# Optimization experiments

Hardware: AMD Instinct MI355X
Metric: run time of the kernel (lower is better)

The kernel has to match this reference:

```python
import jax, jax.numpy as jnp
import numpy as np

MAX_DEGREE = 7  # selected_degree for every neuron (== config.max_degree)


def _cheb_combine(alpha, coeffs):
    """sum_d coeffs[:, d] * T_d(alpha) via the Chebyshev recurrence.

    alpha:  [B, out]
    coeffs: [out, D+1]
    returns [B, out]
    """
    t_m2 = jnp.ones_like(alpha)          # T_0
    t_m1 = alpha                          # T_1
    acc = coeffs[:, 0] + coeffs[:, 1] * alpha

    def body(carry, c_d):                 # c_d: [out]
        tm2, tm1, a = carry
        t = 2.0 * alpha * tm1 - tm2       # T_d recurrence
        return (tm1, t, a + c_d * t), None

    (_, _, acc), _ = jax.lax.scan(body, (t_m2, t_m1, acc), coeffs[:, 2:].T)
    return acc


def _kan_layer(x, w, b, coeffs, cW, cb):
    # w: [out, in] (stacked per-neuron projection vectors), b: [out]
    alpha = x @ w.T + b                   # [B, out] -- per-neuron scalar projection
    neuron_out = _cheb_combine(alpha, coeffs)  # [B, out]
    return neuron_out @ cW + cb           # combine_W [out,out], combin_b [out]


def setup_inputs() -> dict:
    key = jax.random.key(0)
    ks = jax.random.split(key, 12)
    B = 16384
    shape = [1024, 1024, 256]
    D1 = MAX_DEGREE + 1
    inp = {"x": jax.random.normal(ks[0], (B, shape[0]), dtype=jnp.float32)}
    ki = 1
    for li, (din, dout) in enumerate(zip(shape[:-1], shape[1:]), start=1):
        inp[f"w{li}"] = jax.random.normal(ks[ki], (dout, din), dtype=jnp.float32) / np.sqrt(din); ki += 1
        inp[f"b{li}"] = jnp.zeros((dout,), dtype=jnp.float32)
        inp[f"coeffs{li}"] = jax.random.normal(ks[ki], (dout, D1), dtype=jnp.float32) * 0.1; ki += 1
        inp[f"cW{li}"] = jnp.eye(dout, dtype=jnp.float32)
        inp[f"cb{li}"] = jnp.zeros((dout,), dtype=jnp.float32)
    return inp


def reference(x, w1, b1, coeffs1, cW1, cb1, w2, b2, coeffs2, cW2, cb2):
    h = _kan_layer(x, w1, b1, coeffs1, cW1, cb1)
    return _kan_layer(h, w2, b2, coeffs2, cW2, cb2)
```

## Files before the change

### kernel.cpp

```cpp
#include <hip/hip_runtime.h>


typedef __attribute__((ext_vector_type(8))) short short8;
typedef __attribute__((ext_vector_type(4))) float f32x4;
typedef unsigned short ushort_t;

#define GAS(p) ((const __attribute__((address_space(1))) void*)(p))
#define LAS(p) ((__attribute__((address_space(3))) void*)(p))

__device__ __forceinline__ void split2(float f, ushort_t& h, ushort_t& l) {
    const unsigned u = __float_as_uint(f);
    h = (ushort_t)(u >> 16);
    const float hf = __uint_as_float(u & 0xFFFF0000u);
    l = (ushort_t)(__float_as_uint(f - hf) >> 16);
}

__global__ __launch_bounds__(256)
void fused_split(const float* __restrict__ x, ushort_t* __restrict__ xh, ushort_t* __restrict__ xl,
                 const float* __restrict__ w1, ushort_t* __restrict__ w1h, ushort_t* __restrict__ w1l) {
    const int bid = blockIdx.x;
    const float* src; ushort_t* hi; ushort_t* lo; int i;
    if (bid < 16384) { src = x;  hi = xh;  lo = xl;  i = bid * 256 + threadIdx.x; }
    else             { src = w1; hi = w1h; lo = w1l; i = (bid - 16384) * 256 + threadIdx.x; }
    const float4 v = ((const float4*)src)[i];
    ushort4 h, l;
    split2(v.x, h.x, l.x); split2(v.y, h.y, l.y);
    split2(v.z, h.z, l.z); split2(v.w, h.w, l.w);
    ((ushort4*)hi)[i] = h;
    ((ushort4*)lo)[i] = l;
}

constexpr int PKT = 16;
__global__ __launch_bounds__(256)
void prep_gemm_sk(const float* __restrict__ A, const float* __restrict__ W,
                  float* __restrict__ Cp, int M, int N, int K, int KS) {
    __shared__ float As[PKT][68];
    __shared__ float Bs[PKT][68];
    const int tid = threadIdx.x;
    const int bn = blockIdx.x, bm = blockIdx.y, bz = blockIdx.z;
    const int kc = K / KS, k0 = bz * kc;
    const int tx = tid & 15, ty = tid >> 4;
    float acc[4][4];
#pragma unroll
    for (int i = 0; i < 4; ++i)
#pragma unroll
        for (int j = 0; j < 4; ++j) acc[i][j] = 0.f;
    const float* Ab = A + (size_t)(bm * 64) * K + k0;
    const float* Wb = W + (size_t)(bn * 64) * K + k0;
    const int sr = tid >> 2;
    const int sc = (tid & 3) * 4;
    for (int kt = 0; kt < kc; kt += PKT) {
        const float4 va = *(const float4*)(Ab + (size_t)sr * K + kt + sc);
        As[sc + 0][sr] = va.x; As[sc + 1][sr] = va.y; As[sc + 2][sr] = va.z; As[sc + 3][sr] = va.w;
        const float4 vb = *(const float4*)(Wb + (size_t)sr * K + kt + sc);
        Bs[sc + 0][sr] = vb.x; Bs[sc + 1][sr] = vb.y; Bs[sc + 2][sr] = vb.z; Bs[sc + 3][sr] = vb.w;
        __syncthreads();
#pragma unroll
        for (int k = 0; k < PKT; ++k) {
            const float4 a4 = *(const float4*)&As[k][ty * 4];
            const float4 b4 = *(const float4*)&Bs[k][tx * 4];
            const float a[4] = {a4.x, a4.y, a4.z, a4.w};
            const float b[4] = {b4.x, b4.y, b4.z, b4.w};
#pragma unroll
            for (int i = 0; i < 4; ++i)
#pragma unroll
                for (int j = 0; j < 4; ++j) acc[i][j] = fmaf(a[i], b[j], acc[i][j]);
        }
        __syncthreads();
    }
    float* Cb = Cp + (size_t)bz * M * N + (size_t)(bm * 64 + ty * 4) * N + bn * 64 + tx * 4;
#pragma unroll
    for (int i = 0; i < 4; ++i)
        *(float4*)(Cb + (size_t)i * N) = make_float4(acc[i][0], acc[i][1], acc[i][2], acc[i][3]);
}

__global__ __launch_bounds__(256)
void prep_small(const float* __restrict__ m2p, ushort_t* __restrict__ m2h, ushort_t* __restrict__ m2l,
                const float* __restrict__ cW2, ushort_t* __restrict__ cw2h, ushort_t* __restrict__ cw2l,
                const float* __restrict__ cb1, const float* __restrict__ w2,
                const float* __restrict__ b2, float* __restrict__ b2e) {
    const int bid = blockIdx.x;
    if (bid < 256) {
        const int i = bid * 256 + threadIdx.x;
        float4 s = ((const float4*)m2p)[i];
#pragma unroll
        for (int z = 1; z < 4; ++z) {
            const float4 v = ((const float4*)m2p)[(size_t)z * 65536 + i];
            s.x += v.x; s.y += v.y; s.z += v.z; s.w += v.w;
        }
        ushort4 h, l;
        split2(s.x, h.x, l.x); split2(s.y, h.y, l.y);
        split2(s.z, h.z, l.z); split2(s.w, h.w, l.w);
        ((ushort4*)m2h)[i] = h;
        ((ushort4*)m2l)[i] = l;
    } else if (bid < 512) {
        const int i = (bid - 256) * 256 + threadIdx.x;
        const int r = i >> 8, c = i & 255;
        ushort_t h, l;
        split2(cW2[r * 256 + c], h, l);
        cw2h[c * 256 + r] = h;
        cw2l[c * 256 + r] = l;
    } else {
        const int wave = threadIdx.x >> 6, lane = threadIdx.x & 63;
        const int n = (bid - 512) * 4 + wave;
        const float4* row = (const float4*)(w2 + (size_t)n * 1024);
        const float4* c4  = (const float4*)cb1;
        float s = 0.f;
#pragma unroll
        for (int i = 0; i < 4; ++i) {
            const int idx = lane + i * 64;
            const float4 a = row[idx], c = c4[idx];
            s += a.x * c.x + a.y * c.y + a.z * c.z + a.w * c.w;
        }
#pragma unroll
        for (int off = 32; off; off >>= 1) s += __shfl_down(s, off);
        if (lane == 0) b2e[n] = s + b2[n];
    }
}

__global__ __launch_bounds__(512, 2)
void kan_mfma256(const ushort_t* __restrict__ Ahg,
                 const ushort_t* __restrict__ Alg,
                 const ushort_t* __restrict__ Bhg,
                 const ushort_t* __restrict__ Blg,
                 const float* __restrict__ bias,
                 const float* __restrict__ coeffs,
                 ushort_t* __restrict__ Chh,
                 ushort_t* __restrict__ Chl,
                 int M, int N, int K)
{
    __shared__ __align__(16) ushort_t LDS[2][4][256 * 32];

    const int tid  = threadIdx.x;
    const int lane = tid & 63;
    const int wave = tid >> 6;

    const int gx  = gridDim.x;
    const int nwg = gx * gridDim.y;
    int wg = blockIdx.y * gx + blockIdx.x;
    wg = (wg & 7) * (nwg >> 3) + (wg >> 3);
    const int bn = wg % gx;
    const int bm = wg / gx;

    const int wm = wave >> 2;
    const int wn = wave & 3;
    const int lr = lane & 15;
    const int lg = lane >> 4;

    const int sg  = wave & 3;
    const int r0a = (wave >> 2) * 128;
    const size_t aRow0 = (size_t)bm * 256;
    const size_t bRow0 = (size_t)bn * 256;

    f32x4 acc[8][4];
#pragma unroll
    for (int m = 0; m < 8; ++m)
#pragma unroll
        for (int n = 0; n < 4; ++n) acc[m][n] = f32x4{0.f, 0.f, 0.f, 0.f};

    auto stage = [&](int s, int kt) {
#pragma unroll
        for (int rc = 0; rc < 2; ++rc) {
            const int r0 = r0a + rc * 64;
            const size_t ga = (aRow0 + r0 + lane) * K + kt + sg * 8;
            const size_t gb = (bRow0 + r0 + lane) * K + kt + sg * 8;
            const int di = sg * 2048 + r0 * 8;
            __builtin_amdgcn_global_load_lds(GAS(Ahg + ga), LAS(&LDS[s][0][di]), 16, 0, 0);
            __builtin_amdgcn_global_load_lds(GAS(Alg + ga), LAS(&LDS[s][1][di]), 16, 0, 0);
            __builtin_amdgcn_global_load_lds(GAS(Bhg + gb), LAS(&LDS[s][2][di]), 16, 0, 0);
            __builtin_amdgcn_global_load_lds(GAS(Blg + gb), LAS(&LDS[s][3][di]), 16, 0, 0);
        }
    };

    stage(0, 0);
    asm volatile("s_waitcnt vmcnt(0)" ::: "memory");
    __builtin_amdgcn_s_barrier();

    const int nt = K >> 5;

#define CLUSTER256(MH)                                                          \
    {                                                                           \
        short8 ah[4], al4[4];                                                   \
        _Pragma("unroll")                                                       \
        for (int m = 0; m < 4; ++m) {                                           \
            const int idx = lg * 2048 + (wm * 128 + (MH) * 64 + m * 16 + lr) * 8;\
            ah[m]  = *(const short8*)&LDS[cur][0][idx];                         \
            al4[m] = *(const short8*)&LDS[cur][1][idx];                         \
        }                                                                       \
        asm volatile("s_waitcnt lgkmcnt(0)" ::: "memory");                      \
        __builtin_amdgcn_sched_barrier(0);                                      \
        __builtin_amdgcn_s_setprio(1);                                          \
        _Pragma("unroll")                                                       \
        for (int m = 0; m < 4; ++m)                                             \
            _Pragma("unroll")                                                   \
            for (int n = 0; n < 4; ++n) {                                       \
                acc[(MH)*4+m][n] = __builtin_amdgcn_mfma_f32_16x16x32_bf16(ah[m],  bh[n], acc[(MH)*4+m][n], 0, 0, 0); \
                acc[(MH)*4+m][n] = __builtin_amdgcn_mfma_f32_16x16x32_bf16(ah[m],  bl[n], acc[(MH)*4+m][n], 0, 0, 0); \
                acc[(MH)*4+m][n] = __builtin_amdgcn_mfma_f32_16x16x32_bf16(al4[m], bh[n], acc[(MH)*4+m][n], 0, 0, 0); \
            }                                                                   \
        __builtin_amdgcn_s_setprio(0);                                          \
    }

    for (int t = 0; t < nt; ++t) {
        const int cur = t & 1;
        const bool more = (t + 1) < nt;

        if (more) stage(cur ^ 1, (t + 1) << 5);

        short8 bh[4], bl[4];
#pragma unroll
        for (int n = 0; n < 4; ++n) {
            const int idx = lg * 2048 + (wn * 64 + n * 16 + lr) * 8;
            bh[n] = *(const short8*)&LDS[cur][2][idx];
            bl[n] = *(const short8*)&LDS[cur][3][idx];
        }
        CLUSTER256(0)
        CLUSTER256(1)

        if (more) {
            asm volatile("s_waitcnt vmcnt(0)" ::: "memory");
            __builtin_amdgcn_s_barrier();
        }
    }
#undef CLUSTER256

    const int gm0 = bm * 256 + wm * 128;
    const int gn0 = bn * 256 + wn * 64;
#pragma unroll
    for (int n = 0; n < 4; ++n) {
        const int colg = gn0 + n * 16 + lr;
        const float bia = bias[colg];
        float cf[8];
        {
            const float4 u0 = *(const float4*)(coeffs + (size_t)colg * 8);
            const float4 u1 = *(const float4*)(coeffs + (size_t)colg * 8 + 4);
            cf[0] = u0.x; cf[1] = u0.y; cf[2] = u0.z; cf[3] = u0.w;
            cf[4] = u1.x; cf[5] = u1.y; cf[6] = u1.z; cf[7] = u1.w;
        }
#pragma unroll
        for (int m = 0; m < 8; ++m) {
            const int rowb = gm0 + m * 16 + lg * 4;
#pragma unroll
            for (int j = 0; j < 4; ++j) {
                const float alpha = acc[m][n][j] + bia;
                float tm2 = 1.f, tm1 = alpha;
                float v = fmaf(cf[1], alpha, cf[0]);
#pragma unroll
                for (int d = 2; d < 8; ++d) {
                    const float tch = 2.f * alpha * tm1 - tm2;
                    v = fmaf(cf[d], tch, v);
                    tm2 = tm1; tm1 = tch;
                }
                const size_t o = (size_t)(rowb + j) * N + colg;
                ushort_t h, l2;
                split2(v, h, l2);
                Chh[o] = h; Chl[o] = l2;
            }
        }
    }
}

template<bool CHEB, bool OUT_F32>
__global__ __launch_bounds__(256, 2)
void kan_mfma(const ushort_t* __restrict__ Ahg,
              const ushort_t* __restrict__ Alg,
              const ushort_t* __restrict__ Bhg,
              const ushort_t* __restrict__ Blg,
              const float* __restrict__ bias,
              const float* __restrict__ coeffs,
              float* __restrict__ Cf,
              ushort_t* __restrict__ Chh,
              ushort_t* __restrict__ Chl,
              int M, int N, int K)
{
    __shared__ __align__(16) ushort_t LDS[2][4][128 * 32];

    const int tid  = threadIdx.x;
    const int lane = tid & 63;
    const int wave = tid >> 6;

    const int gx = gridDim.x;
    const int nwg = gx * gridDim.y;
    int wg = blockIdx.y * gx + blockIdx.x;
    wg = (wg & 7) * (nwg >> 3) + (wg >> 3);
    const int bn = wg % gx;
    const int bm = wg / gx;

    const int wm = wave >> 1, wn = wave & 1;
    const int lr = lane & 15;
    const int lg = lane >> 4;

    f32x4 acc[4][4];
#pragma unroll
    for (int m = 0; m < 4; ++m)
#pragma unroll
        for (int n = 0; n < 4; ++n) acc[m][n] = f32x4{0.f, 0.f, 0.f, 0.f};

    const size_t aRow0 = (size_t)(bm * 128);
    const size_t bRow0 = (size_t)(bn * 128);
    const int sg = wave;
    const int ldsb = sg * 1024;

    auto stage = [&](int s, int kt) {
#pragma unroll
        for (int rc = 0; rc < 2; ++rc) {
            const int r0 = rc * 64;
            const size_t ga = (aRow0 + r0 + lane) * K + kt + sg * 8;
            const size_t gb = (bRow0 + r0 + lane) * K + kt + sg * 8;
            const int di = ldsb + r0 * 8;
            __builtin_amdgcn_global_load_lds(GAS(Ahg + ga), LAS(&LDS[s][0][di]), 16, 0, 0);
            __builtin_amdgcn_global_load_lds(GAS(Alg + ga), LAS(&LDS[s][1][di]), 16, 0, 0);
            __builtin_amdgcn_global_load_lds(GAS(Bhg + gb), LAS(&LDS[s][2][di]), 16, 0, 0);
            __builtin_amdgcn_global_load_lds(GAS(Blg + gb), LAS(&LDS[s][3][di]), 16, 0, 0);
        }
    };

    stage(0, 0);
    asm volatile("s_waitcnt vmcnt(0)" ::: "memory");
    __builtin_amdgcn_s_barrier();

    const int nt = K >> 5;
    for (int t = 0; t < nt; ++t) {
        const int cur = t & 1;
        const bool more = (t + 1) < nt;

        if (more) stage(cur ^ 1, (t + 1) << 5);

        short8 a_h[4], a_l[4], b_h[4], b_l[4];
#pragma unroll
        for (int m = 0; m < 4; ++m) {
            const int off = lg * 1024 + (wm * 64 + m * 16 + lr) * 8;
            a_h[m] = *(const short8*)&LDS[cur][0][off];
            a_l[m] = *(const short8*)&LDS[cur][1][off];
        }
#pragma unroll
        for (int n = 0; n < 4; ++n) {
            const int off = lg * 1024 + (wn * 64 + n * 16 + lr) * 8;
            b_h[n] = *(const short8*)&LDS[cur][2][off];
            b_l[n] = *(const short8*)&LDS[cur][3][off];
        }
        asm volatile("s_waitcnt lgkmcnt(0)" ::: "memory");
        __builtin_amdgcn_sched_barrier(0);
        __builtin_amdgcn_s_setprio(1);
#pragma unroll
        for (int m = 0; m < 4; ++m)
#pragma unroll
            for (int n = 0; n < 4; ++n) {
                acc[m][n] = __builtin_amdgcn_mfma_f32_16x16x32_bf16(a_h[m], b_h[n], acc[m][n], 0, 0, 0);
                acc[m][n] = __builtin_amdgcn_mfma_f32_16x16x32_bf16(a_h[m], b_l[n], acc[m][n], 0, 0, 0);
                acc[m][n] = __builtin_amdgcn_mfma_f32_16x16x32_bf16(a_l[m], b_h[n], acc[m][n], 0, 0, 0);
            }
        __builtin_amdgcn_s_setprio(0);

        if (more) {
            asm volatile("s_waitcnt vmcnt(0)" ::: "memory");
            __builtin_amdgcn_s_barrier();
        }
    }

    const int gm0 = bm * 128 + wm * 64;
    const int gn0 = bn * 128 + wn * 64;
#pragma unroll
    for (int n = 0; n < 4; ++n) {
        const int colg = gn0 + n * 16 + lr;
        const float bia = bias[colg];
        float cf[8];
        if constexpr (CHEB) {
            const float4 u0 = *(const float4*)(coeffs + (size_t)colg * 8);
            const float4 u1 = *(const float4*)(coeffs + (size_t)colg * 8 + 4);
            cf[0] = u0.x; cf[1] = u0.y; cf[2] = u0.z; cf[3] = u0.w;
            cf[4] = u1.x; cf[5] = u1.y; cf[6] = u1.z; cf[7] = u1.w;
        }
#pragma unroll
        for (int m = 0; m < 4; ++m) {
            const int rowb = gm0 + m * 16 + lg * 4;
#pragma unroll
            for (int j = 0; j < 4; ++j) {
                const float alpha = acc[m][n][j] + bia;
                float v;
                if constexpr (CHEB) {
                    float tm2 = 1.f, tm1 = alpha;
                    v = fmaf(cf[1], alpha, cf[0]);
#pragma unroll
                    for (int d = 2; d < 8; ++d) {
                        const float t2 = 2.f * alpha * tm1 - tm2;
                        v = fmaf(cf[d], t2, v);
                        tm2 = tm1; tm1 = t2;
                    }
                } else {
                    v = alpha;
                }
                const size_t o = (size_t)(rowb + j) * N + colg;
                if constexpr (OUT_F32) {
                    Cf[o] = v;
                } else {
                    ushort_t h, l2;
                    split2(v, h, l2);
                    Chh[o] = h; Chl[o] = l2;
                }
            }
        }
    }
}

extern "C" void kernel_launch(void* const* d_in, const int* in_sizes, int n_in,
                              void* d_out, int out_size, void* d_ws, size_t ws_size,
                              hipStream_t stream) {
    const float* x       = (const float*)d_in[0];
    const float* w1      = (const float*)d_in[1];
    const float* b1      = (const float*)d_in[2];
    const float* coeffs1 = (const float*)d_in[3];
    const float* cW1     = (const float*)d_in[4];
    const float* cb1     = (const float*)d_in[5];
    const float* w2      = (const float*)d_in[6];
    const float* b2      = (const float*)d_in[7];
    const float* coeffs2 = (const float*)d_in[8];
    const float* cW2     = (const float*)d_in[9];
    const float* cb2     = (const float*)d_in[10];

    constexpr int B  = 16384;
    constexpr int D1 = 1024;
    constexpr int D2 = 256;
    constexpr int KS = 4;

    char* w = (char*)d_ws;
    size_t off = 0;
    auto alloc = [&](size_t bytes) { char* p = w + off; off += (bytes + 255) & ~(size_t)255; return p; };
    ushort_t* xh   = (ushort_t*)alloc((size_t)B * D1 * 2);
    ushort_t* xl   = (ushort_t*)alloc((size_t)B * D1 * 2);
    ushort_t* hh   = (ushort_t*)alloc((size_t)B * D1 * 2);
    ushort_t* hl   = (ushort_t*)alloc((size_t)B * D1 * 2);
    ushort_t* ph   = (ushort_t*)alloc((size_t)B * D2 * 2);
    ushort_t* pl   = (ushort_t*)alloc((size_t)B * D2 * 2);
    ushort_t* w1h  = (ushort_t*)alloc((size_t)D1 * D1 * 2);
    ushort_t* w1l  = (ushort_t*)alloc((size_t)D1 * D1 * 2);
    float*    m2p  = (float*)alloc((size_t)KS * D2 * D1 * 4);
    ushort_t* m2h  = (ushort_t*)alloc((size_t)D2 * D1 * 2);
    ushort_t* m2l  = (ushort_t*)alloc((size_t)D2 * D1 * 2);
    ushort_t* cw2h = (ushort_t*)alloc((size_t)D2 * D2 * 2);
    ushort_t* cw2l = (ushort_t*)alloc((size_t)D2 * D2 * 2);
    float*    b2e  = (float*)alloc(D2 * 4);

    fused_split<<<dim3(B * D1 / 4 / 256 + D1 * D1 / 4 / 256), dim3(256), 0, stream>>>(
        x, xh, xl, w1, w1h, w1l);
    prep_gemm_sk<<<dim3(D1 / 64, D2 / 64, KS), dim3(256), 0, stream>>>(w2, cW1, m2p, D2, D1, D1, KS);
    prep_small<<<dim3(576), dim3(256), 0, stream>>>(m2p, m2h, m2l, cW2, cw2h, cw2l, cb1, w2, b2, b2e);

    kan_mfma256<<<dim3(D1 / 256, B / 256), dim3(512), 0, stream>>>(
        xh, xl, w1h, w1l, b1, coeffs1, hh, hl, B, D1, D1);
    kan_mfma<true, false><<<dim3(D2 / 128, B / 128), dim3(256), 0, stream>>>(
        hh, hl, m2h, m2l, b2e, coeffs2, nullptr, ph, pl, B, D2, D1);
    kan_mfma<false, true><<<dim3(D2 / 128, B / 128), dim3(256), 0, stream>>>(
        ph, pl, cw2h, cw2l, cb2, nullptr, (float*)d_out, nullptr, nullptr, B, D2, D2);
}
```

Baseline: 339.3 us.

## Fuse x hi/lo split into first GEMM and pack intermediates as interleaved u32

```diff
diff --git a/kernel.cpp b/kernel.cpp
--- a/kernel.cpp
+++ b/kernel.cpp
@@ -3,6 +3,7 @@
 
 typedef __attribute__((ext_vector_type(8))) short short8;
 typedef __attribute__((ext_vector_type(4))) float f32x4;
+typedef __attribute__((ext_vector_type(4))) unsigned uint32x4;
 typedef unsigned short ushort_t;
 
 #define GAS(p) ((const __attribute__((address_space(1))) void*)(p))
@@ -13,21 +14,6 @@
     h = (ushort_t)(u >> 16);
     const float hf = __uint_as_float(u & 0xFFFF0000u);
     l = (ushort_t)(__float_as_uint(f - hf) >> 16);
-}
-
-__global__ __launch_bounds__(256)
-void fused_split(const float* __restrict__ x, ushort_t* __restrict__ xh, ushort_t* __restrict__ xl,
-                 const float* __restrict__ w1, ushort_t* __restrict__ w1h, ushort_t* __restrict__ w1l) {
-    const int bid = blockIdx.x;
-    const float* src; ushort_t* hi; ushort_t* lo; int i;
-    if (bid < 16384) { src = x;  hi = xh;  lo = xl;  i = bid * 256 + threadIdx.x; }
-    else             { src = w1; hi = w1h; lo = w1l; i = (bid - 16384) * 256 + threadIdx.x; }
-    const float4 v = ((const float4*)src)[i];
-    ushort4 h, l;
-    split2(v.x, h.x, l.x); split2(v.y, h.y, l.y);
-    split2(v.z, h.z, l.z); split2(v.w, h.w, l.w);
-    ((ushort4*)hi)[i] = h;
-    ((ushort4*)lo)[i] = l;
 }
 
 constexpr int PKT = 16;
@@ -75,13 +61,22 @@
 }
 
 __global__ __launch_bounds__(256)
-void prep_small(const float* __restrict__ m2p, ushort_t* __restrict__ m2h, ushort_t* __restrict__ m2l,
-                const float* __restrict__ cW2, ushort_t* __restrict__ cw2h, ushort_t* __restrict__ cw2l,
-                const float* __restrict__ cb1, const float* __restrict__ w2,
-                const float* __restrict__ b2, float* __restrict__ b2e) {
+void prep_all(const float* __restrict__ w1, ushort_t* __restrict__ w1h, ushort_t* __restrict__ w1l,
+              const float* __restrict__ m2p, ushort_t* __restrict__ m2h, ushort_t* __restrict__ m2l,
+              const float* __restrict__ cW2, ushort_t* __restrict__ cw2h, ushort_t* __restrict__ cw2l,
+              const float* __restrict__ cb1, const float* __restrict__ w2,
+              const float* __restrict__ b2, float* __restrict__ b2e) {
     const int bid = blockIdx.x;
-    if (bid < 256) {
+    if (bid < 1024) {
         const int i = bid * 256 + threadIdx.x;
+        const float4 v = ((const float4*)w1)[i];
+        ushort4 h, l;
+        split2(v.x, h.x, l.x); split2(v.y, h.y, l.y);
+        split2(v.z, h.z, l.z); split2(v.w, h.w, l.w);
+        ((ushort4*)w1h)[i] = h;
+        ((ushort4*)w1l)[i] = l;
+    } else if (bid < 1280) {
+        const int i = (bid - 1024) * 256 + threadIdx.x;
         float4 s = ((const float4*)m2p)[i];
 #pragma unroll
         for (int z = 1; z < 4; ++z) {
@@ -93,8 +88,8 @@
         split2(s.z, h.z, l.z); split2(s.w, h.w, l.w);
         ((ushort4*)m2h)[i] = h;
         ((ushort4*)m2l)[i] = l;
-    } else if (bid < 512) {
-        const int i = (bid - 256) * 256 + threadIdx.x;
+    } else if (bid < 1536) {
+        const int i = (bid - 1280) * 256 + threadIdx.x;
         const int r = i >> 8, c = i & 255;
         ushort_t h, l;
         split2(cW2[r * 256 + c], h, l);
@@ -102,7 +97,7 @@
         cw2l[c * 256 + r] = l;
     } else {
         const int wave = threadIdx.x >> 6, lane = threadIdx.x & 63;
-        const int n = (bid - 512) * 4 + wave;
+        const int n = (bid - 1536) * 4 + wave;
         const float4* row = (const float4*)(w2 + (size_t)n * 1024);
         const float4* c4  = (const float4*)cb1;
         float s = 0.f;
@@ -119,17 +114,16 @@
 }
 
 __global__ __launch_bounds__(512, 2)
-void kan_mfma256(const ushort_t* __restrict__ Ahg,
-                 const ushort_t* __restrict__ Alg,
-                 const ushort_t* __restrict__ Bhg,
-                 const ushort_t* __restrict__ Blg,
-                 const float* __restrict__ bias,
-                 const float* __restrict__ coeffs,
-                 ushort_t* __restrict__ Chh,
-                 ushort_t* __restrict__ Chl,
-                 int M, int N, int K)
+void kan_g1(const float* __restrict__ Xf,
+            const ushort_t* __restrict__ Bhg,
+            const ushort_t* __restrict__ Blg,
+            const float* __restrict__ bias,
+            const float* __restrict__ coeffs,
+            unsigned* __restrict__ Cpk,
+            int M, int N, int K)
 {
-    __shared__ __align__(16) ushort_t LDS[2][4][256 * 32];
+    __shared__ __align__(16) float    Asf[2][4][2][256 * 4];
+    __shared__ __align__(16) ushort_t Bsh[2][2][4][256 * 8];
 
     const int tid  = threadIdx.x;
     const int lane = tid & 63;
@@ -158,71 +152,76 @@
 #pragma unroll
         for (int n = 0; n < 4; ++n) acc[m][n] = f32x4{0.f, 0.f, 0.f, 0.f};
 
-    auto stage = [&](int s, int kt) {
-#pragma unroll
-        for (int rc = 0; rc < 2; ++rc) {
-            const int r0 = r0a + rc * 64;
-            const size_t ga = (aRow0 + r0 + lane) * K + kt + sg * 8;
-            const size_t gb = (bRow0 + r0 + lane) * K + kt + sg * 8;
-            const int di = sg * 2048 + r0 * 8;
-            __builtin_amdgcn_global_load_lds(GAS(Ahg + ga), LAS(&LDS[s][0][di]), 16, 0, 0);
-            __builtin_amdgcn_global_load_lds(GAS(Alg + ga), LAS(&LDS[s][1][di]), 16, 0, 0);
-            __builtin_amdgcn_global_load_lds(GAS(Bhg + gb), LAS(&LDS[s][2][di]), 16, 0, 0);
-            __builtin_amdgcn_global_load_lds(GAS(Blg + gb), LAS(&LDS[s][3][di]), 16, 0, 0);
-        }
+    auto stageA = [&](int s, int kt) {
+#pragma unroll
+        for (int rc = 0; rc < 2; ++rc)
+#pragma unroll
+            for (int h = 0; h < 2; ++h) {
+                const int r0 = r0a + rc * 64;
+                const float* src = Xf + (aRow0 + r0 + lane) * (size_t)K + kt + sg * 8 + h * 4;
+                __builtin_amdgcn_global_load_lds(GAS(src), LAS(&Asf[s][sg][h][r0 * 4]), 16, 0, 0);
+            }
     };
-
-    stage(0, 0);
+    auto stageB = [&](int s, int kt) {
+#pragma unroll
+        for (int rc = 0; rc < 2; ++rc)
+#pragma unroll
+            for (int hl = 0; hl < 2; ++hl) {
+                const int r0 = r0a + rc * 64;
+                const ushort_t* src = (hl ? Blg : Bhg) + (bRow0 + r0 + lane) * (size_t)K + kt + sg * 8;
+                __builtin_amdgcn_global_load_lds(GAS(src), LAS(&Bsh[s][hl][sg][r0 * 8]), 16, 0, 0);
+            }
+    };
+
+    stageA(0, 0); stageB(0, 0);
     asm volatile("s_waitcnt vmcnt(0)" ::: "memory");
-    __builtin_amdgcn_s_barrier();
+    __syncthreads();
 
     const int nt = K >> 5;
-
-#define CLUSTER256(MH)                                                          \
-    {                                                                           \
-        short8 ah[4], al4[4];                                                   \
-        _Pragma("unroll")                                                       \
-        for (int m = 0; m < 4; ++m) {                                           \
-            const int idx = lg * 2048 + (wm * 128 + (MH) * 64 + m * 16 + lr) * 8;\
-            ah[m]  = *(const short8*)&LDS[cur][0][idx];                         \
-            al4[m] = *(const short8*)&LDS[cur][1][idx];                         \
-        }                                                                       \
-        asm volatile("s_waitcnt lgkmcnt(0)" ::: "memory");                      \
-        __builtin_amdgcn_sched_barrier(0);                                      \
-        __builtin_amdgcn_s_setprio(1);                                          \
-        _Pragma("unroll")                                                       \
-        for (int m = 0; m < 4; ++m)                                             \
-            _Pragma("unroll")                                                   \
-            for (int n = 0; n < 4; ++n) {                                       \
-                acc[(MH)*4+m][n] = __builtin_amdgcn_mfma_f32_16x16x32_bf16(ah[m],  bh[n], acc[(MH)*4+m][n], 0, 0, 0); \
-                acc[(MH)*4+m][n] = __builtin_amdgcn_mfma_f32_16x16x32_bf16(ah[m],  bl[n], acc[(MH)*4+m][n], 0, 0, 0); \
-                acc[(MH)*4+m][n] = __builtin_amdgcn_mfma_f32_16x16x32_bf16(al4[m], bh[n], acc[(MH)*4+m][n], 0, 0, 0); \
-            }                                                                   \
-        __builtin_amdgcn_s_setprio(0);                                          \
-    }
-
     for (int t = 0; t < nt; ++t) {
         const int cur = t & 1;
         const bool more = (t + 1) < nt;
 
-        if (more) stage(cur ^ 1, (t + 1) << 5);
+        if (more) { stageA(cur ^ 1, (t + 1) << 5); stageB(cur ^ 1, (t + 1) << 5); }
 
         short8 bh[4], bl[4];
 #pragma unroll
         for (int n = 0; n < 4; ++n) {
-            const int idx = lg * 2048 + (wn * 64 + n * 16 + lr) * 8;
-            bh[n] = *(const short8*)&LDS[cur][2][idx];
-            bl[n] = *(const short8*)&LDS[cur][3][idx];
-        }
-        CLUSTER256(0)
-        CLUSTER256(1)
+            const int row = wn * 64 + n * 16 + lr;
+            bh[n] = *(const short8*)&Bsh[cur][0][lg][row * 8];
+            bl[n] = *(const short8*)&Bsh[cur][1][lg][row * 8];
+        }
+#pragma unroll
+        for (int half = 0; half < 2; ++half) {
+            short8 ah[4], al[4];
+#pragma unroll
+            for (int m = 0; m < 4; ++m) {
+                const int row = wm * 128 + (half * 4 + m) * 16 + lr;
+                const f32x4 lo4 = *(const f32x4*)&Asf[cur][lg][0][row * 4];
+                const f32x4 hi4 = *(const f32x4*)&Asf[cur][lg][1][row * 4];
+#pragma unroll
+                for (int e = 0; e < 4; ++e) {
+                    ushort_t h, l;
+                    split2(lo4[e], h, l); ah[m][e] = (short)h;     al[m][e] = (short)l;
+                    split2(hi4[e], h, l); ah[m][4 + e] = (short)h; al[m][4 + e] = (short)l;
+                }
+            }
+#pragma unroll
+            for (int m = 0; m < 4; ++m)
+#pragma unroll
+                for (int n = 0; n < 4; ++n) {
+                    const int am = half * 4 + m;
+                    acc[am][n] = __builtin_amdgcn_mfma_f32_16x16x32_bf16(ah[m], bh[n], acc[am][n], 0, 0, 0);
+                    acc[am][n] = __builtin_amdgcn_mfma_f32_16x16x32_bf16(ah[m], bl[n], acc[am][n], 0, 0, 0);
+                    acc[am][n] = __builtin_amdgcn_mfma_f32_16x16x32_bf16(al[m], bh[n], acc[am][n], 0, 0, 0);
+                }
+        }
 
         if (more) {
             asm volatile("s_waitcnt vmcnt(0)" ::: "memory");
-            __builtin_amdgcn_s_barrier();
-        }
-    }
-#undef CLUSTER256
+            __syncthreads();
+        }
+    }
 
     const int gm0 = bm * 256 + wm * 128;
     const int gn0 = bn * 256 + wn * 64;
@@ -251,10 +250,9 @@
                     v = fmaf(cf[d], tch, v);
                     tm2 = tm1; tm1 = tch;
                 }
-                const size_t o = (size_t)(rowb + j) * N + colg;
                 ushort_t h, l2;
                 split2(v, h, l2);
-                Chh[o] = h; Chl[o] = l2;
+                Cpk[(size_t)(rowb + j) * N + colg] = ((unsigned)h << 16) | l2;
             }
         }
     }
@@ -262,18 +260,17 @@
 
 template<bool CHEB, bool OUT_F32>
 __global__ __launch_bounds__(256, 2)
-void kan_mfma(const ushort_t* __restrict__ Ahg,
-              const ushort_t* __restrict__ Alg,
-              const ushort_t* __restrict__ Bhg,
-              const ushort_t* __restrict__ Blg,
-              const float* __restrict__ bias,
-              const float* __restrict__ coeffs,
-              float* __restrict__ Cf,
-              ushort_t* __restrict__ Chh,
-              ushort_t* __restrict__ Chl,
-              int M, int N, int K)
+void kan_pk(const unsigned* __restrict__ Apg,
+            const ushort_t* __restrict__ Bhg,
+            const ushort_t* __restrict__ Blg,
+            const float* __restrict__ bias,
+            const float* __restrict__ coeffs,
+            float* __restrict__ Cf,
+            unsigned* __restrict__ Cpk,
+            int M, int N, int K)
 {
-    __shared__ __align__(16) ushort_t LDS[2][4][128 * 32];
+    __shared__ __align__(16) unsigned Apk[2][4][2][128 * 4];
+    __shared__ __align__(16) ushort_t Bsh[2][2][4][128 * 8];
 
     const int tid  = threadIdx.x;
     const int lane = tid & 63;
@@ -299,25 +296,27 @@
     const size_t aRow0 = (size_t)(bm * 128);
     const size_t bRow0 = (size_t)(bn * 128);
     const int sg = wave;
-    const int ldsb = sg * 1024;
 
     auto stage = [&](int s, int kt) {
 #pragma unroll
         for (int rc = 0; rc < 2; ++rc) {
             const int r0 = rc * 64;
-            const size_t ga = (aRow0 + r0 + lane) * K + kt + sg * 8;
-            const size_t gb = (bRow0 + r0 + lane) * K + kt + sg * 8;
-            const int di = ldsb + r0 * 8;
-            __builtin_amdgcn_global_load_lds(GAS(Ahg + ga), LAS(&LDS[s][0][di]), 16, 0, 0);
-            __builtin_amdgcn_global_load_lds(GAS(Alg + ga), LAS(&LDS[s][1][di]), 16, 0, 0);
-            __builtin_amdgcn_global_load_lds(GAS(Bhg + gb), LAS(&LDS[s][2][di]), 16, 0, 0);
-            __builtin_amdgcn_global_load_lds(GAS(Blg + gb), LAS(&LDS[s][3][di]), 16, 0, 0);
+#pragma unroll
+            for (int h = 0; h < 2; ++h) {
+                const unsigned* srcA = Apg + (aRow0 + r0 + lane) * (size_t)K + kt + sg * 8 + h * 4;
+                __builtin_amdgcn_global_load_lds(GAS(srcA), LAS(&Apk[s][sg][h][r0 * 4]), 16, 0, 0);
+            }
+#pragma unroll
+            for (int hl = 0; hl < 2; ++hl) {
+                const ushort_t* srcB = (hl ? Blg : Bhg) + (bRow0 + r0 + lane) * (size_t)K + kt + sg * 8;
+                __builtin_amdgcn_global_load_lds(GAS(srcB), LAS(&Bsh[s][hl][sg][r0 * 8]), 16, 0, 0);
+            }
         }
     };
 
     stage(0, 0);
     asm volatile("s_waitcnt vmcnt(0)" ::: "memory");
-    __builtin_amdgcn_s_barrier();
+    __syncthreads();
 
     const int nt = K >> 5;
     for (int t = 0; t < nt; ++t) {
@@ -326,35 +325,37 @@
 
         if (more) stage(cur ^ 1, (t + 1) << 5);
 
-        short8 a_h[4], a_l[4], b_h[4], b_l[4];
+        short8 bh[4], bl[4];
+#pragma unroll
+        for (int n = 0; n < 4; ++n) {
+            const int row = wn * 64 + n * 16 + lr;
+            bh[n] = *(const short8*)&Bsh[cur][0][lg][row * 8];
+            bl[n] = *(const short8*)&Bsh[cur][1][lg][row * 8];
+        }
+        short8 ah[4], al[4];
 #pragma unroll
         for (int m = 0; m < 4; ++m) {
-            const int off = lg * 1024 + (wm * 64 + m * 16 + lr) * 8;
-            a_h[m] = *(const short8*)&LDS[cur][0][off];
-            a_l[m] = *(const short8*)&LDS[cur][1][off];
-        }
-#pragma unroll
-        for (int n = 0; n < 4; ++n) {
-            const int off = lg * 1024 + (wn * 64 + n * 16 + lr) * 8;
-            b_h[n] = *(const short8*)&LDS[cur][2][off];
-            b_l[n] = *(const short8*)&LDS[cur][3][off];
-        }
-        asm volatile("s_waitcnt lgkmcnt(0)" ::: "memory");
-        __builtin_amdgcn_sched_barrier(0);
-        __builtin_amdgcn_s_setprio(1);
+            const int row = wm * 64 + m * 16 + lr;
+            const uint32x4 lo4 = *(const uint32x4*)&Apk[cur][lg][0][row * 4];
+            const uint32x4 hi4 = *(const uint32x4*)&Apk[cur][lg][1][row * 4];
+#pragma unroll
+            for (int e = 0; e < 4; ++e) {
+                ah[m][e]     = (short)(lo4[e] >> 16); al[m][e]     = (short)(lo4[e] & 0xFFFFu);
+                ah[m][4 + e] = (short)(hi4[e] >> 16); al[m][4 + e] = (short)(hi4[e] & 0xFFFFu);
+            }
+        }
 #pragma unroll
         for (int m = 0; m < 4; ++m)
 #pragma unroll
             for (int n = 0; n < 4; ++n) {
-                acc[m][n] = __builtin_amdgcn_mfma_f32_16x16x32_bf16(a_h[m], b_h[n], acc[m][n], 0, 0, 0);
-                acc[m][n] = __builtin_amdgcn_mfma_f32_16x16x32_bf16(a_h[m], b_l[n], acc[m][n], 0, 0, 0);
-                acc[m][n] = __builtin_amdgcn_mfma_f32_16x16x32_bf16(a_l[m], b_h[n], acc[m][n], 0, 0, 0);
-            }
-        __builtin_amdgcn_s_setprio(0);
+                acc[m][n] = __builtin_amdgcn_mfma_f32_16x16x32_bf16(ah[m], bh[n], acc[m][n], 0, 0, 0);
+                acc[m][n] = __builtin_amdgcn_mfma_f32_16x16x32_bf16(ah[m], bl[n], acc[m][n], 0, 0, 0);
+                acc[m][n] = __builtin_amdgcn_mfma_f32_16x16x32_bf16(al[m], bh[n], acc[m][n], 0, 0, 0);
+            }
 
         if (more) {
             asm volatile("s_waitcnt vmcnt(0)" ::: "memory");
-            __builtin_amdgcn_s_barrier();
+            __syncthreads();
         }
     }
 
@@ -396,7 +397,7 @@
                 } else {
                     ushort_t h, l2;
                     split2(v, h, l2);
-                    Chh[o] = h; Chl[o] = l2;
+                    Cpk[o] = ((unsigned)h << 16) | l2;
                 }
             }
         }
@@ -426,12 +427,8 @@
     char* w = (char*)d_ws;
     size_t off = 0;
     auto alloc = [&](size_t bytes) { char* p = w + off; off += (bytes + 255) & ~(size_t)255; return p; };
-    ushort_t* xh   = (ushort_t*)alloc((size_t)B * D1 * 2);
-    ushort_t* xl   = (ushort_t*)alloc((size_t)B * D1 * 2);
-    ushort_t* hh   = (ushort_t*)alloc((size_t)B * D1 * 2);
-    ushort_t* hl   = (ushort_t*)alloc((size_t)B * D1 * 2);
-    ushort_t* ph   = (ushort_t*)alloc((size_t)B * D2 * 2);
-    ushort_t* pl   = (ushort_t*)alloc((size_t)B * D2 * 2);
+    unsigned* hp   = (unsigned*)alloc((size_t)B * D1 * 4);
+    unsigned* ppk  = (unsigned*)alloc((size_t)B * D2 * 4);
     ushort_t* w1h  = (ushort_t*)alloc((size_t)D1 * D1 * 2);
     ushort_t* w1l  = (ushort_t*)alloc((size_t)D1 * D1 * 2);
     float*    m2p  = (float*)alloc((size_t)KS * D2 * D1 * 4);
@@ -441,15 +438,14 @@
     ushort_t* cw2l = (ushort_t*)alloc((size_t)D2 * D2 * 2);
     float*    b2e  = (float*)alloc(D2 * 4);
 
-    fused_split<<<dim3(B * D1 / 4 / 256 + D1 * D1 / 4 / 256), dim3(256), 0, stream>>>(
-        x, xh, xl, w1, w1h, w1l);
     prep_gemm_sk<<<dim3(D1 / 64, D2 / 64, KS), dim3(256), 0, stream>>>(w2, cW1, m2p, D2, D1, D1, KS);
-    prep_small<<<dim3(576), dim3(256), 0, stream>>>(m2p, m2h, m2l, cW2, cw2h, cw2l, cb1, w2, b2, b2e);
-
-    kan_mfma256<<<dim3(D1 / 256, B / 256), dim3(512), 0, stream>>>(
-        xh, xl, w1h, w1l, b1, coeffs1, hh, hl, B, D1, D1);
-    kan_mfma<true, false><<<dim3(D2 / 128, B / 128), dim3(256), 0, stream>>>(
-        hh, hl, m2h, m2l, b2e, coeffs2, nullptr, ph, pl, B, D2, D1);
-    kan_mfma<false, true><<<dim3(D2 / 128, B / 128), dim3(256), 0, stream>>>(
-        ph, pl, cw2h, cw2l, cb2, nullptr, (float*)d_out, nullptr, nullptr, B, D2, D2);
-}
+    prep_all<<<dim3(1600), dim3(256), 0, stream>>>(w1, w1h, w1l, m2p, m2h, m2l,
+                                                   cW2, cw2h, cw2l, cb1, w2, b2, b2e);
+
+    kan_g1<<<dim3(D1 / 256, B / 256), dim3(512), 0, stream>>>(
+        x, w1h, w1l, b1, coeffs1, hp, B, D1, D1);
+    kan_pk<true, false><<<dim3(D2 / 128, B / 128), dim3(256), 0, stream>>>(
+        hp, m2h, m2l, b2e, coeffs2, nullptr, ppk, B, D2, D1);
+    kan_pk<false, true><<<dim3(D2 / 128, B / 128), dim3(256), 0, stream>>>(
+        ppk, cw2h, cw2l, cb2, nullptr, (float*)d_out, nullptr, B, D2, D2);
+}
```

After: 343.6 us. Within noise of the previous version (+1.3%).
